# Kernel optimization log

Measured on AMD Instinct MI355X. Metric: run time of the kernel, lower is better.

Reference implementation:

```python
import jax, jax.numpy as jnp
import numpy as np

IN_F, OUT_F, RANK = 4096, 4096, 8
TOKENS = 8192


def setup_inputs() -> dict:
    key = jax.random.key(0)
    k1, k2, k3 = jax.random.split(key, 3)
    x = jax.random.normal(k1, (TOKENS, IN_F), dtype=jnp.float32)
    # xavier-uniform-ish init scale for the TT cores
    lim0 = float(np.sqrt(6.0 / (OUT_F + RANK)))
    lim1 = float(np.sqrt(6.0 / (RANK + IN_F)))
    core0 = jax.random.uniform(k2, (1, OUT_F, RANK), minval=-lim0, maxval=lim0, dtype=jnp.float32)
    core1 = jax.random.uniform(k3, (RANK, IN_F, 1), minval=-lim1, maxval=lim1, dtype=jnp.float32)
    bias = jnp.zeros((OUT_F,), dtype=jnp.float32)
    return {"x": x, "core0": core0, "core1": core1, "bias": bias}


def reference(x, core0, core1, bias):
    # Faithful to torch: weight[o, i] = sum_r core0[0, o, r] * core1[r, i, 0]
    # (original einsum 'ior, ri1 -> oi' with the size-1 leading/trailing dims broadcast)
    weight = jnp.einsum('or,ri->oi', core0[0], core1[:, :, 0])  # [OUT_F, IN_F]
    # F.linear: x @ weight.T + bias
    return x @ weight.T + bias
```

## Files before the change

### kernel.cpp

```cpp
#include <hip/hip_runtime.h>


#define TOKENS 8192
#define IN_F   4096
#define OUT_F  4096
#define RANK   8
#define TB     8

typedef float f32x4 __attribute__((ext_vector_type(4)));

__global__ __launch_bounds__(256) void tt_fused(const float* __restrict__ x,
                                                const float* __restrict__ core0,
                                                const float* __restrict__ core1,
                                                const float* __restrict__ bias,
                                                float* __restrict__ out) {
    __shared__ __align__(16) float y_lds[TB][RANK];

    const int tid  = threadIdx.x;
    const int wave = tid >> 6;
    const int lane = tid & 63;
    const int tblk = blockIdx.x * TB;
    const int t0   = tblk + wave * 2;

    const float* x0 = x + (size_t)t0 * IN_F;
    const float* x1 = x0 + IN_F;

    float acc0[RANK], acc1[RANK];
    #pragma unroll
    for (int r = 0; r < RANK; ++r) { acc0[r] = 0.f; acc1[r] = 0.f; }

    #pragma unroll 4
    for (int k = 0; k < 16; ++k) {
        const int i = 4 * (lane + 64 * k);
        const f32x4 a0 = __builtin_nontemporal_load((const f32x4*)(x0 + i));
        const f32x4 a1 = __builtin_nontemporal_load((const f32x4*)(x1 + i));
        #pragma unroll
        for (int r = 0; r < RANK; ++r) {
            const f32x4 c = *(const f32x4*)(core1 + r * IN_F + i);
            acc0[r] += a0.x * c.x + a0.y * c.y + a0.z * c.z + a0.w * c.w;
            acc1[r] += a1.x * c.x + a1.y * c.y + a1.z * c.z + a1.w * c.w;
        }
    }

    #pragma unroll
    for (int r = 0; r < RANK; ++r) {
        #pragma unroll
        for (int off = 32; off > 0; off >>= 1) {
            acc0[r] += __shfl_xor(acc0[r], off, 64);
            acc1[r] += __shfl_xor(acc1[r], off, 64);
        }
    }

    if (lane == 0) {
        f32x4* yp0 = (f32x4*)&y_lds[wave * 2 + 0][0];
        f32x4* yp1 = (f32x4*)&y_lds[wave * 2 + 1][0];
        yp0[0] = (f32x4){acc0[0], acc0[1], acc0[2], acc0[3]};
        yp0[1] = (f32x4){acc0[4], acc0[5], acc0[6], acc0[7]};
        yp1[0] = (f32x4){acc1[0], acc1[1], acc1[2], acc1[3]};
        yp1[1] = (f32x4){acc1[4], acc1[5], acc1[6], acc1[7]};
    }
    __syncthreads();

    #pragma unroll 1
    for (int og = 0; og < 4; ++og) {
        const int o = og * 1024 + tid * 4;
        f32x4 w[8];
        #pragma unroll
        for (int j = 0; j < 4; ++j) {
            w[2 * j]     = *(const f32x4*)(core0 + (o + j) * RANK);
            w[2 * j + 1] = *(const f32x4*)(core0 + (o + j) * RANK + 4);
        }
        const f32x4 b = *(const f32x4*)(bias + o);

        #pragma unroll
        for (int t = 0; t < TB; ++t) {
            const f32x4 y0 = *(const f32x4*)(&y_lds[t][0]);
            const f32x4 y1 = *(const f32x4*)(&y_lds[t][4]);
            f32x4 c;
            c.x = b.x + y0.x * w[0].x + y0.y * w[0].y + y0.z * w[0].z + y0.w * w[0].w
                      + y1.x * w[1].x + y1.y * w[1].y + y1.z * w[1].z + y1.w * w[1].w;
            c.y = b.y + y0.x * w[2].x + y0.y * w[2].y + y0.z * w[2].z + y0.w * w[2].w
                      + y1.x * w[3].x + y1.y * w[3].y + y1.z * w[3].z + y1.w * w[3].w;
            c.z = b.z + y0.x * w[4].x + y0.y * w[4].y + y0.z * w[4].z + y0.w * w[4].w
                      + y1.x * w[5].x + y1.y * w[5].y + y1.z * w[5].z + y1.w * w[5].w;
            c.w = b.w + y0.x * w[6].x + y0.y * w[6].y + y0.z * w[6].z + y0.w * w[6].w
                      + y1.x * w[7].x + y1.y * w[7].y + y1.z * w[7].z + y1.w * w[7].w;
            __builtin_nontemporal_store(c, (f32x4*)(out + (size_t)(tblk + t) * OUT_F + o));
        }
    }
}

extern "C" void kernel_launch(void* const* d_in, const int* in_sizes, int n_in,
                              void* d_out, int out_size, void* d_ws, size_t ws_size,
                              hipStream_t stream) {
    const float* x     = (const float*)d_in[0];
    const float* core0 = (const float*)d_in[1];
    const float* core1 = (const float*)d_in[2];
    const float* bias  = (const float*)d_in[3];
    float* out = (float*)d_out;
    (void)d_ws; (void)ws_size;

    tt_fused<<<TOKENS / TB, 256, 0, stream>>>(x, core0, core1, bias, out);
}
```

Baseline: 251.2 us.

## Split IN_F reduction across wave pairs with four tokens per wave

Each wave now handles four tokens over half of the input dimension instead of two tokens over the full dimension. Every core1 vector load is reused across four tokens rather than two, halving core1 traffic per token. Partial rank sums from the two halves go to shared memory and are added during the output phase. This costs more accumulator registers (32 vs 16) and more shuffle reductions per wave.

```diff
diff --git a/kernel.cpp b/kernel.cpp
--- a/kernel.cpp
+++ b/kernel.cpp
@@ -14,50 +14,56 @@
                                                 const float* __restrict__ core1,
                                                 const float* __restrict__ bias,
                                                 float* __restrict__ out) {
-    __shared__ __align__(16) float y_lds[TB][RANK];
+    __shared__ __align__(16) float y_part[4][4][RANK];
 
-    const int tid  = threadIdx.x;
-    const int wave = tid >> 6;
-    const int lane = tid & 63;
-    const int tblk = blockIdx.x * TB;
-    const int t0   = tblk + wave * 2;
+    const int tid   = threadIdx.x;
+    const int wave  = tid >> 6;
+    const int lane  = tid & 63;
+    const int tblk  = blockIdx.x * TB;
+    const int tg    = wave >> 1;
+    const int ih    = wave & 1;
+    const int ibase = ih * (IN_F / 2);
 
-    const float* x0 = x + (size_t)t0 * IN_F;
-    const float* x1 = x0 + IN_F;
+    const float* xb = x + (size_t)(tblk + tg * 4) * IN_F + ibase;
+    const float* cb = core1 + ibase;
 
-    float acc0[RANK], acc1[RANK];
+    float acc[4][RANK];
     #pragma unroll
-    for (int r = 0; r < RANK; ++r) { acc0[r] = 0.f; acc1[r] = 0.f; }
+    for (int t = 0; t < 4; ++t)
+        #pragma unroll
+        for (int r = 0; r < RANK; ++r) acc[t][r] = 0.f;
 
     #pragma unroll 4
-    for (int k = 0; k < 16; ++k) {
+    for (int k = 0; k < 8; ++k) {
         const int i = 4 * (lane + 64 * k);
-        const f32x4 a0 = __builtin_nontemporal_load((const f32x4*)(x0 + i));
-        const f32x4 a1 = __builtin_nontemporal_load((const f32x4*)(x1 + i));
+        f32x4 a[4];
+        #pragma unroll
+        for (int t = 0; t < 4; ++t)
+            a[t] = __builtin_nontemporal_load((const f32x4*)(xb + (size_t)t * IN_F + i));
         #pragma unroll
         for (int r = 0; r < RANK; ++r) {
-            const f32x4 c = *(const f32x4*)(core1 + r * IN_F + i);
-            acc0[r] += a0.x * c.x + a0.y * c.y + a0.z * c.z + a0.w * c.w;
-            acc1[r] += a1.x * c.x + a1.y * c.y + a1.z * c.z + a1.w * c.w;
+            const f32x4 c = *(const f32x4*)(cb + r * IN_F + i);
+            #pragma unroll
+            for (int t = 0; t < 4; ++t)
+                acc[t][r] += a[t].x * c.x + a[t].y * c.y + a[t].z * c.z + a[t].w * c.w;
         }
     }
 
     #pragma unroll
-    for (int r = 0; r < RANK; ++r) {
+    for (int t = 0; t < 4; ++t)
         #pragma unroll
-        for (int off = 32; off > 0; off >>= 1) {
-            acc0[r] += __shfl_xor(acc0[r], off, 64);
-            acc1[r] += __shfl_xor(acc1[r], off, 64);
-        }
-    }
+        for (int r = 0; r < RANK; ++r)
+            #pragma unroll
+            for (int off = 32; off > 0; off >>= 1)
+                acc[t][r] += __shfl_xor(acc[t][r], off, 64);
 
     if (lane == 0) {
-        f32x4* yp0 = (f32x4*)&y_lds[wave * 2 + 0][0];
-        f32x4* yp1 = (f32x4*)&y_lds[wave * 2 + 1][0];
-        yp0[0] = (f32x4){acc0[0], acc0[1], acc0[2], acc0[3]};
-        yp0[1] = (f32x4){acc0[4], acc0[5], acc0[6], acc0[7]};
-        yp1[0] = (f32x4){acc1[0], acc1[1], acc1[2], acc1[3]};
-        yp1[1] = (f32x4){acc1[4], acc1[5], acc1[6], acc1[7]};
+        #pragma unroll
+        for (int t = 0; t < 4; ++t) {
+            f32x4* yp = (f32x4*)&y_part[wave][t][0];
+            yp[0] = (f32x4){acc[t][0], acc[t][1], acc[t][2], acc[t][3]};
+            yp[1] = (f32x4){acc[t][4], acc[t][5], acc[t][6], acc[t][7]};
+        }
     }
     __syncthreads();
 
@@ -74,8 +80,12 @@
 
         #pragma unroll
         for (int t = 0; t < TB; ++t) {
-            const f32x4 y0 = *(const f32x4*)(&y_lds[t][0]);
-            const f32x4 y1 = *(const f32x4*)(&y_lds[t][4]);
+            const int g  = t >> 2;
+            const int tl = t & 3;
+            const f32x4 y0 = *(const f32x4*)&y_part[2 * g][tl][0]
+                           + *(const f32x4*)&y_part[2 * g + 1][tl][0];
+            const f32x4 y1 = *(const f32x4*)&y_part[2 * g][tl][4]
+                           + *(const f32x4*)&y_part[2 * g + 1][tl][4];
             f32x4 c;
             c.x = b.x + y0.x * w[0].x + y0.y * w[0].y + y0.z * w[0].z + y0.w * w[0].w
                       + y1.x * w[1].x + y1.y * w[1].y + y1.z * w[1].z + y1.w * w[1].w;
```

Measured after the change: 248.2 us. About the same (-1.2%).
